# Optimization experiments

Hardware: AMD Instinct MI355X
Metric: run time of the kernel (lower is better)

Reference implementation:

```python
import jax, jax.numpy as jnp
import numpy as np

N = 50000
E = 800000
F_IN = 128
HID = 64
HEADS = 4
P = 16384


def setup_inputs() -> dict:
    key = jax.random.key(0)
    ks = jax.random.split(key, 20)
    s = 0.05
    inp = {
        'x': jax.random.normal(ks[0], (N, F_IN), jnp.float32),
        'edge_src': jax.random.randint(ks[1], (E,), 0, N, jnp.int32),
        'edge_dst': jax.random.randint(ks[2], (E,), 0, N, jnp.int32),
        'edge_attr': jax.random.uniform(ks[3], (E, 1), jnp.float32),
        'pair_indices': jax.random.randint(ks[4], (P, 2), 0, N, jnp.int32),
        # conv1: in=F_IN, heads=4, out=HID, edge_dim=1
        'W1': jax.random.normal(ks[5], (F_IN, HEADS * HID), jnp.float32) * s,
        'We1': jax.random.normal(ks[6], (1, HEADS * HID), jnp.float32) * s,
        'as1': jax.random.normal(ks[7], (HEADS, HID), jnp.float32) * s,
        'ad1': jax.random.normal(ks[8], (HEADS, HID), jnp.float32) * s,
        'ae1': jax.random.normal(ks[9], (HEADS, HID), jnp.float32) * s,
        'b1': jnp.zeros((HEADS * HID,), jnp.float32),
        # conv2: in=4*HID, heads=1, out=HID
        'W2': jax.random.normal(ks[10], (HEADS * HID, HID), jnp.float32) * s,
        'We2': jax.random.normal(ks[11], (1, HID), jnp.float32) * s,
        'as2': jax.random.normal(ks[12], (1, HID), jnp.float32) * s,
        'ad2': jax.random.normal(ks[13], (1, HID), jnp.float32) * s,
        'ae2': jax.random.normal(ks[14], (1, HID), jnp.float32) * s,
        'b2': jnp.zeros((HID,), jnp.float32),
        'Wlin': jax.random.normal(ks[15], (2 * HID, 1), jnp.float32) * s,
        'blin': jnp.zeros((1,), jnp.float32),
    }
    return inp


def gat_conv(x, src, dst, edge_attr, W, We, att_src, att_dst, att_edge, bias, heads, C):
    """PyG GATConv (add_self_loops=True, fill_value='mean', negative_slope=0.2, eval mode)."""
    n = x.shape[0]
    # self-loop edge_attr = mean of incoming edge attrs per node
    deg = jax.ops.segment_sum(jnp.ones_like(dst, dtype=edge_attr.dtype), dst, num_segments=n)
    loop_attr = jax.ops.segment_sum(edge_attr, dst, num_segments=n) / jnp.maximum(deg, 1.0)[:, None]
    loop = jnp.arange(n, dtype=src.dtype)
    src_f = jnp.concatenate([src, loop])
    dst_f = jnp.concatenate([dst, loop])
    ea = jnp.concatenate([edge_attr, loop_attr], axis=0)  # [E+N, 1]
    h = (x @ W).reshape(n, heads, C)                      # [N, H, C]
    a_src = (h * att_src).sum(-1)                         # [N, H]
    a_dst = (h * att_dst).sum(-1)
    e = (ea @ We).reshape(-1, heads, C)                   # [E+N, H, C]
    a_edge = (e * att_edge).sum(-1)                       # [E+N, H]
    alpha = jax.nn.leaky_relu(a_src[src_f] + a_dst[dst_f] + a_edge, 0.2)
    amax = jax.ops.segment_max(alpha, dst_f, num_segments=n)
    ex = jnp.exp(alpha - amax[dst_f])
    denom = jax.ops.segment_sum(ex, dst_f, num_segments=n)
    w = ex / denom[dst_f]                                 # segment softmax over dst
    msg = h[src_f] * w[..., None]                         # [E+N, H, C]
    out = jax.ops.segment_sum(msg, dst_f, num_segments=n) # [N, H, C]
    return out.reshape(n, heads * C) + bias


def reference(x, edge_src, edge_dst, edge_attr, pair_indices,
              W1, We1, as1, ad1, ae1, b1,
              W2, We2, as2, ad2, ae2, b2, Wlin, blin):
    # dropout is identity in eval mode
    h1 = jax.nn.elu(gat_conv(x, edge_src, edge_dst, edge_attr,
                             W1, We1, as1, ad1, ae1, b1, HEADS, HID))
    h2 = gat_conv(h1, edge_src, edge_dst, edge_attr,
                  W2, We2, as2, ad2, ae2, b2, 1, HID)
    d1 = h2[pair_indices[:, 0]]
    d2 = h2[pair_indices[:, 1]]
    pf = jnp.concatenate([d1, d2], axis=1)                # [P, 2*HID]
    return jax.nn.sigmoid(pf @ Wlin + blin).reshape(-1)
```

## Files before the change

kernel.cpp:

```cpp
#include <hip/hip_runtime.h>
#include <hip/hip_fp16.h>
#include <math.h>

typedef __attribute__((ext_vector_type(8))) short short8;
typedef __attribute__((ext_vector_type(4))) float floatx4;
typedef __attribute__((ext_vector_type(2))) float float2v;

#define LOG2E 1.4426950408889634f

__device__ __forceinline__ unsigned short f2bf(float f){
  unsigned int x = __float_as_uint(f);
  unsigned int r = x + 0x7fff + ((x >> 16) & 1);
  return (unsigned short)(r >> 16);
}
__device__ __forceinline__ unsigned cvtpkbf(float lo, float hi){
  unsigned r;
  asm("v_cvt_pk_bf16_f32 %0, %1, %2" : "=v"(r) : "v"(lo), "v"(hi));
  return r;
}
__device__ __forceinline__ short8 pk8(float4 a0, float4 a1){
  unsigned t[4];
  t[0] = cvtpkbf(a0.x, a0.y); t[1] = cvtpkbf(a0.z, a0.w);
  t[2] = cvtpkbf(a1.x, a1.y); t[3] = cvtpkbf(a1.z, a1.w);
  short8 r; __builtin_memcpy(&r, t, 16); return r;
}
__device__ __forceinline__ unsigned char f2fp8(float v){
  int pk = __builtin_amdgcn_cvt_pk_fp8_f32(v, 0.f, 0, false);
  return (unsigned char)(pk & 0xff);
}
__device__ __forceinline__ float wsumf(float v){
#pragma unroll
  for (int o = 32; o; o >>= 1) v += __shfl_xor(v, o, 64);
  return v;
}
__device__ __forceinline__ unsigned pkh2(float a, float b){
  auto p = __builtin_amdgcn_cvt_pkrtz(a, b);
  unsigned u; __builtin_memcpy(&u, &p, 4); return u;
}
__device__ __forceinline__ float h2f(unsigned v){
  unsigned short us = (unsigned short)v;
  __fp16 h; __builtin_memcpy(&h, &us, 2);
  return (float)h;
}

__global__ __launch_bounds__(64) void k_prep(
    const float* __restrict__ W1, const float* __restrict__ as1,
    const float* __restrict__ ad1, const float* __restrict__ W2,
    const float* __restrict__ as2, const float* __restrict__ ad2,
    const float* __restrict__ We1, const float* __restrict__ ae1,
    const float* __restrict__ We2, const float* __restrict__ ae2,
    const float* __restrict__ b2, const float* __restrict__ Wlin,
    unsigned short* __restrict__ W1p, float* __restrict__ w2vT,
    float* __restrict__ ce){
  int b = blockIdx.x, lane = threadIdx.x;
  if (b < 68){
    int nt = b >> 2, kc = b & 3;
    int col = lane & 15, krow = kc * 32 + (lane >> 4) * 8;
    unsigned short tmp[8];
    if (nt < 16){
#pragma unroll
      for (int j = 0; j < 8; j++) tmp[j] = f2bf(W1[(size_t)(krow + j) * 256 + nt * 16 + col]);
    } else {
#pragma unroll
      for (int j = 0; j < 8; j++){
        float v = 0.f;
        if (col < 8){
          const float* av = (col < 4) ? as1 : ad1;
          int h = col & 3;
          for (int c = 0; c < 64; c++)
            v += W1[(size_t)(krow + j) * 256 + h * 64 + c] * av[h * 64 + c];
          v *= LOG2E;
        }
        tmp[j] = f2bf(v);
      }
    }
    unsigned short* dstp = W1p + (((size_t)nt * 4 + kc) * 64 + lane) * 8;
    *(ushort4*)(dstp)     = make_ushort4(tmp[0], tmp[1], tmp[2], tmp[3]);
    *(ushort4*)(dstp + 4) = make_ushort4(tmp[4], tmp[5], tmp[6], tmp[7]);
  } else if (b < 72){
    int k = (b - 68) * 64 + lane;
    float4 a = make_float4(0.f, 0.f, 0.f, 0.f);
    for (int c = 0; c < 64; c++){
      float wv = W2[(size_t)k * 64 + c];
      a.x += wv * as2[c];
      a.y += wv * ad2[c];
      a.z += wv * Wlin[c];
      a.w += wv * Wlin[64 + c];
    }
    w2vT[k]       = a.x * LOG2E;
    w2vT[256 + k] = a.y * LOG2E;
    w2vT[512 + k] = a.z;
    w2vT[768 + k] = a.w;
  } else {
    float p0 = We1[lane]       * ae1[lane];
    float p1 = We1[64 + lane]  * ae1[64 + lane];
    float p2 = We1[128 + lane] * ae1[128 + lane];
    float p3 = We1[192 + lane] * ae1[192 + lane];
    float p4 = We2[lane]       * ae2[lane];
    float c1 = b2[lane] * Wlin[lane];
    float c2 = b2[lane] * Wlin[64 + lane];
    p0 = wsumf(p0); p1 = wsumf(p1); p2 = wsumf(p2); p3 = wsumf(p3); p4 = wsumf(p4);
    c1 = wsumf(c1); c2 = wsumf(c2);
    if (lane == 0){
      ce[0] = p0 * LOG2E; ce[1] = p1 * LOG2E; ce[2] = p2 * LOG2E; ce[3] = p3 * LOG2E;
      ce[4] = p4 * LOG2E;
      ce[5] = c1; ce[6] = c2;
    }
  }
}

__global__ __launch_bounds__(256, 2) void k_count_gemm(
    const int* __restrict__ dst, const float* __restrict__ eattr,
    unsigned* __restrict__ degp, unsigned char* __restrict__ rank,
    int E, int N, int gbl,
    const float* __restrict__ A, const unsigned short* __restrict__ Bp,
    unsigned char* __restrict__ h1f8, float* __restrict__ asrc,
    float* __restrict__ adst, int M){
  __shared__ unsigned short Bs[256 * 64];
  if ((int)blockIdx.x >= gbl){
    int eb = blockIdx.x - gbl;
    int e0 = eb * 512 + threadIdx.x;
    int e1 = e0 + 256;
    bool v0 = e0 < E, v1 = e1 < E;
    int d0 = 0, d1 = 0; float a0 = 0.f, a1 = 0.f;
    if (v0){ d0 = dst[e0]; a0 = eattr[e0]; }
    if (v1){ d1 = dst[e1]; a1 = eattr[e1]; }
    int b0 = (e0 >> 8) & 7, b1 = (e1 >> 8) & 7;
    if (v0){
      unsigned old = atomicAdd(&degp[(size_t)b0 * N + d0],
                               (1u << 24) | (unsigned)(a0 * 262144.0f));
      rank[e0] = (unsigned char)(old >> 24);
    }
    if (v1){
      unsigned old = atomicAdd(&degp[(size_t)b1 * N + d1],
                               (1u << 24) | (unsigned)(a1 * 262144.0f));
      rank[e1] = (unsigned char)(old >> 24);
    }
    return;
  }
  constexpr int K = 128, NKC = 4;
  int wave = threadIdx.x >> 6, lane = threadIdx.x & 63;
  int quad = lane >> 4, col = lane & 15;
  int r0a = blockIdx.x * 128 + wave * 16;
  int r0b = r0a + 64;
  int rowa = min(r0a + col, M - 1);
  int rowb = min(r0b + col, M - 1);
  short8 afa[NKC], afb[NKC], sf[NKC];
#pragma unroll
  for (int kc = 0; kc < NKC; kc++){
    float4 a0 = *(const float4*)(A + (size_t)rowa * K + kc * 32 + quad * 8);
    float4 a1 = *(const float4*)(A + (size_t)rowa * K + kc * 32 + quad * 8 + 4);
    float4 b0 = *(const float4*)(A + (size_t)rowb * K + kc * 32 + quad * 8);
    float4 b1 = *(const float4*)(A + (size_t)rowb * K + kc * 32 + quad * 8 + 4);
    afa[kc] = pk8(a0, a1);
    afb[kc] = pk8(b0, b1);
    sf[kc] = *(const short8*)(Bp + (((size_t)16 * 4 + kc) * 64 + lane) * 8);
  }
  floatx4 acc0[17], acc1[17];
#pragma unroll
  for (int nt = 0; nt < 17; nt++){
    acc0[nt] = (floatx4){0.f, 0.f, 0.f, 0.f};
    acc1[nt] = (floatx4){0.f, 0.f, 0.f, 0.f};
  }
#pragma unroll
  for (int ph = 0; ph < 2; ph++){
    {
      const uint4* srcp = (const uint4*)(Bp + ph * 16384);
      uint4* dstp = (uint4*)Bs;
      for (int i = threadIdx.x; i < 2048; i += 256) dstp[i] = srcp[i];
    }
    __syncthreads();
#pragma unroll
    for (int kc = 0; kc < NKC; kc++){
#pragma unroll
      for (int t = 0; t < 8; t++){
        short8 bfv = *(const short8*)(&Bs[((t * NKC + kc) * 64 + lane) * 8]);
        acc0[ph * 8 + t] = __builtin_amdgcn_mfma_f32_16x16x32_bf16(afa[kc], bfv, acc0[ph * 8 + t], 0, 0, 0);
        acc1[ph * 8 + t] = __builtin_amdgcn_mfma_f32_16x16x32_bf16(afb[kc], bfv, acc1[ph * 8 + t], 0, 0, 0);
      }
    }
    __syncthreads();
  }
#pragma unroll
  for (int kc = 0; kc < NKC; kc++){
    acc0[16] = __builtin_amdgcn_mfma_f32_16x16x32_bf16(afa[kc], sf[kc], acc0[16], 0, 0, 0);
    acc1[16] = __builtin_amdgcn_mfma_f32_16x16x32_bf16(afb[kc], sf[kc], acc1[16], 0, 0, 0);
  }
#pragma unroll
  for (int nt = 0; nt < 16; nt++){
#pragma unroll
    for (int i = 0; i < 4; i++){
      int r = r0a + quad * 4 + i;
      if (r < M) h1f8[(size_t)r * 256 + nt * 16 + col] = f2fp8(acc0[nt][i]);
    }
  }
#pragma unroll
  for (int i = 0; i < 4; i++){
    int r = r0a + quad * 4 + i;
    if (r < M){
      float v = acc0[16][i];
      if (col < 4)      asrc[(size_t)r * 4 + col] = v;
      else if (col < 8) adst[(size_t)r * 4 + (col - 4)] = v;
    }
  }
#pragma unroll
  for (int nt = 0; nt < 16; nt++){
#pragma unroll
    for (int i = 0; i < 4; i++){
      int r = r0b + quad * 4 + i;
      if (r < M) h1f8[(size_t)r * 256 + nt * 16 + col] = f2fp8(acc1[nt][i]);
    }
  }
#pragma unroll
  for (int i = 0; i < 4; i++){
    int r = r0b + quad * 4 + i;
    if (r < M){
      float v = acc1[16][i];
      if (col < 4)      asrc[(size_t)r * 4 + col] = v;
      else if (col < 8) adst[(size_t)r * 4 + (col - 4)] = v;
    }
  }
}

__global__ __launch_bounds__(256) void k_scan1(const unsigned* __restrict__ degp,
    int* __restrict__ row_ptr, int* __restrict__ bsum, int n){
  __shared__ int sm[2][256];
  int tid = threadIdx.x, gid = blockIdx.x * 256 + tid;
  int v = 0;
  if (gid < n){
#pragma unroll
    for (int b = 0; b < 8; b++) v += (int)(degp[(size_t)b * n + gid] >> 24);
  }
  sm[0][tid] = v; __syncthreads();
  int pin = 0;
  for (int off = 1; off < 256; off <<= 1){
    int t = sm[pin][tid];
    if (tid >= off) t += sm[pin][tid - off];
    sm[pin ^ 1][tid] = t; pin ^= 1; __syncthreads();
  }
  int incl = sm[pin][tid];
  if (gid < n) row_ptr[gid] = incl - v;
  if (tid == 255) bsum[blockIdx.x] = incl;
}

__global__ __launch_bounds__(256) void k_scan3(int* __restrict__ row_ptr,
    const int* __restrict__ bsum, const unsigned* __restrict__ degp,
    float* __restrict__ lattr, int* __restrict__ base, int n, int E){
  int tid = threadIdx.x;
  int partial = (tid < (int)blockIdx.x) ? bsum[tid] : 0;
#pragma unroll
  for (int o = 32; o; o >>= 1) partial += __shfl_xor(partial, o, 64);
  __shared__ int ws[4];
  if ((tid & 63) == 0) ws[tid >> 6] = partial;
  __syncthreads();
  int blockOfs = ws[0] + ws[1] + ws[2] + ws[3];
  int gid = blockIdx.x * 256 + tid;
  if (gid >= n) return;
  int rp = row_ptr[gid] + blockOfs;
  row_ptr[gid] = rp;
  int cum = 0; float s = 0.f;
  int bb[8];
#pragma unroll
  for (int b = 0; b < 8; b++){
    unsigned p = degp[(size_t)b * n + gid];
    bb[b] = rp + cum;
    cum += (int)(p >> 24);
    s += (float)(p & 0xffffffu);
  }
  lattr[gid] = (s * (1.0f / 262144.0f)) / fmaxf((float)cum, 1.0f);
  int4* bp = (int4*)(base + (size_t)gid * 8);
  bp[0] = make_int4(bb[0], bb[1], bb[2], bb[3]);
  bp[1] = make_int4(bb[4], bb[5], bb[6], bb[7]);
  if (gid == 0) row_ptr[n] = E;
}

__global__ __launch_bounds__(256) void k_scatter(const int* __restrict__ src,
    const int* __restrict__ dst, const float* __restrict__ eattr,
    const unsigned char* __restrict__ rank, const int* __restrict__ base,
    const float* __restrict__ a_src, int4* __restrict__ csr, int E){
  int e0 = blockIdx.x * 512 + threadIdx.x;
  int e1 = e0 + 256;
  bool v0 = e0 < E, v1 = e1 < E;
  int b0 = (e0 >> 8) & 7, b1 = (e1 >> 8) & 7;
  if (v0){
    int d = dst[e0], s = src[e0];
    int pos = base[(size_t)d * 8 + b0] + (int)rank[e0];
    float4 av = *(const float4*)(a_src + ((size_t)s << 2));
    csr[pos] = make_int4(s, __float_as_int(eattr[e0]),
                         (int)pkh2(av.x, av.y), (int)pkh2(av.z, av.w));
  }
  if (v1){
    int d = dst[e1], s = src[e1];
    int pos = base[(size_t)d * 8 + b1] + (int)rank[e1];
    float4 av = *(const float4*)(a_src + ((size_t)s << 2));
    csr[pos] = make_int4(s, __float_as_int(eattr[e1]),
                         (int)pkh2(av.x, av.y), (int)pkh2(av.z, av.w));
  }
}

__global__ __launch_bounds__(128) void k_gat1(
    const int* __restrict__ row_ptr, const int4* __restrict__ csr,
    const float* __restrict__ lattr,
    const float* __restrict__ a_src, const float* __restrict__ a_dst,
    const float* __restrict__ ce, const unsigned char* __restrict__ hpre,
    const float* __restrict__ bias, const float* __restrict__ w2vT,
    float4* __restrict__ upd, int n){
  int node = blockIdx.x * 2 + (threadIdx.x >> 6);
  if (node >= n) return;
  int lane = threadIdx.x & 63;
  int q = lane >> 4, lsub = lane & 15, hq = lsub >> 2;
  int start = row_ptr[node], deg = row_ptr[node + 1] - start;
  float4 as4 = *(const float4*)(a_src + (size_t)node * 4);
  float4 ad4 = *(const float4*)(a_dst + (size_t)node * 4);
  float4 ce4 = *(const float4*)ce;
  float la = lattr[node];
  float asvh = hq == 0 ? as4.x : hq == 1 ? as4.y : hq == 2 ? as4.z : as4.w;
  float advh = hq == 0 ? ad4.x : hq == 1 ? ad4.y : hq == 2 ? ad4.z : ad4.w;
  float ceh  = hq == 0 ? ce4.x : hq == 1 ? ce4.y : hq == 2 ? ce4.z : ce4.w;
  unsigned lso = (unsigned)(lsub << 4);
  int hsh = (hq & 1) * 16;
  float2v acc2[8];
#pragma unroll
  for (int k = 0; k < 8; k++) acc2[k] = (float2v){0.f, 0.f};
  float dn = 0.f;
  if (q == 0){
    float aself = fmaf(la, ceh, asvh + advh);
    aself = aself > 0.f ? aself : 0.2f * aself;
    float wself = __builtin_amdgcn_exp2f(aself);
    dn = wself;
    uint4 u = *(const uint4*)(hpre + (((unsigned)node << 8) + lso));
    float2v w2 = (float2v){wself, wself};
    unsigned uu[4] = {u.x, u.y, u.z, u.w};
#pragma unroll
    for (int j = 0; j < 4; j++){
      acc2[2 * j]     = w2 * __builtin_amdgcn_cvt_pk_f32_fp8((int)uu[j], false);
      acc2[2 * j + 1] = w2 * __builtin_amdgcn_cvt_pk_f32_fp8((int)uu[j], true);
    }
  }
  int4 sA = make_int4(0, 0, 0, 0), sB;
  if (q < deg) sA = csr[start + q];
  sB = sA;
  if (q + 4 < deg) sB = csr[start + q + 4];
  for (int e = q; e < deg; e += 8){
    uint4 uA = *(const uint4*)(hpre + (((unsigned)sA.x << 8) + lso));
    uint4 uB = *(const uint4*)(hpre + (((unsigned)sB.x << 8) + lso));
    int4 nA = sA, nB;
    int en = e + 8;
    if (en < deg) nA = csr[start + en];
    nB = nA;
    if (en + 4 < deg) nB = csr[start + en + 4];
    bool vB = (e + 4) < deg;
    unsigned hwA = (hq & 2) ? (unsigned)sA.w : (unsigned)sA.z;
    unsigned hwB = (hq & 2) ? (unsigned)sB.w : (unsigned)sB.z;
    float gA = h2f(hwA >> hsh);
    float gB = h2f(hwB >> hsh);
    float aA = fmaf(__int_as_float(sA.y), ceh, gA + advh);
    float aB = fmaf(__int_as_float(sB.y), ceh, gB + advh);
    aA = aA > 0.f ? aA : 0.2f * aA;
    aB = aB > 0.f ? aB : 0.2f * aB;
    float wA = __builtin_amdgcn_exp2f(aA);
    float wB = vB ? __builtin_amdgcn_exp2f(aB) : 0.f;
    dn += wA + wB;
    float2v wA2 = (float2v){wA, wA}, wB2 = (float2v){wB, wB};
    unsigned ua[4] = {uA.x, uA.y, uA.z, uA.w};
    unsigned ub[4] = {uB.x, uB.y, uB.z, uB.w};
#pragma unroll
    for (int j = 0; j < 4; j++){
      acc2[2 * j]     += wA2 * __builtin_amdgcn_cvt_pk_f32_fp8((int)ua[j], false);
      acc2[2 * j + 1] += wA2 * __builtin_amdgcn_cvt_pk_f32_fp8((int)ua[j], true);
      acc2[2 * j]     += wB2 * __builtin_amdgcn_cvt_pk_f32_fp8((int)ub[j], false);
      acc2[2 * j + 1] += wB2 * __builtin_amdgcn_cvt_pk_f32_fp8((int)ub[j], true);
    }
    sA = nA; sB = nB;
  }
  dn += __shfl_xor(dn, 16, 64);
  dn += __shfl_xor(dn, 32, 64);
#pragma unroll
  for (int k = 0; k < 8; k++){
    acc2[k].x += __shfl_xor(acc2[k].x, 16, 64);
    acc2[k].x += __shfl_xor(acc2[k].x, 32, 64);
    acc2[k].y += __shfl_xor(acc2[k].y, 16, 64);
    acc2[k].y += __shfl_xor(acc2[k].y, 32, 64);
  }
  {
    float inv = 1.f / dn;
    float d = 0.f;
#pragma unroll
    for (int j = 0; j < 4; j++){
      float4 b4  = *(const float4*)(bias + lsub * 16 + j * 4);
      float4 wvj = *(const float4*)(w2vT + (size_t)lane * 16 + j * 4);
      float bbv[4] = {b4.x, b4.y, b4.z, b4.w};
      float wvv[4] = {wvj.x, wvj.y, wvj.z, wvj.w};
#pragma unroll
      for (int t = 0; t < 4; t++){
        int k = j * 4 + t;
        float av = (k & 1) ? acc2[k >> 1].y : acc2[k >> 1].x;
        float v = av * inv + bbv[t];
        v = v > 0.f ? v : (__expf(v) - 1.f);
        d += v * wvv[t];
      }
    }
#pragma unroll
    for (int o = 1; o < 16; o <<= 1) d += __shfl_xor(d, o, 64);
    if (lsub == 0) ((float*)&upd[node])[q] = d;
  }
}

__global__ __launch_bounds__(128) void k_gat2(
    const int* __restrict__ row_ptr, const int4* __restrict__ csr,
    const float* __restrict__ lattr, const float4* __restrict__ upd,
    const float* __restrict__ ce,
    float* __restrict__ s1v, float* __restrict__ s2v, int n){
  int node = blockIdx.x * 16 + (threadIdx.x >> 3);
  if (node >= n) return;
  int lane8 = threadIdx.x & 7;
  int start = row_ptr[node], deg = row_ptr[node + 1] - start;
  float4 own = upd[node];
  float ad = own.y, c = ce[4];
  const float* updf = (const float*)upd;
  float t1 = 0.f, t2 = 0.f, dn = 0.f;
  if (lane8 == 0){
    float a = fmaf(lattr[node], c, own.x + ad);
    a = a > 0.f ? a : 0.2f * a;
    float w = __builtin_amdgcn_exp2f(a);
    dn = w; t1 = w * own.z; t2 = w * own.w;
  }
  for (int e = lane8; e < deg; e += 16){
    bool vB = (e + 8) < deg;
    int4 sA = csr[start + e];
    int4 sB = csr[start + (vB ? e + 8 : e)];
    float4 oA = *(const float4*)(updf + ((unsigned)sA.x << 2));
    float4 oB = *(const float4*)(updf + ((unsigned)sB.x << 2));
    float aA = fmaf(__int_as_float(sA.y), c, oA.x + ad);
    float aB = fmaf(__int_as_float(sB.y), c, oB.x + ad);
    aA = aA > 0.f ? aA : 0.2f * aA;
    aB = aB > 0.f ? aB : 0.2f * aB;
    float wA = __builtin_amdgcn_exp2f(aA);
    float wB = vB ? __builtin_amdgcn_exp2f(aB) : 0.f;
    dn += wA + wB;
    t1 = fmaf(wA, oA.z, fmaf(wB, oB.z, t1));
    t2 = fmaf(wA, oA.w, fmaf(wB, oB.w, t2));
  }
#pragma unroll
  for (int o = 1; o < 8; o <<= 1){
    dn += __shfl_xor(dn, o, 64);
    t1 += __shfl_xor(t1, o, 64);
    t2 += __shfl_xor(t2, o, 64);
  }
  if (lane8 == 0){
    float inv = 1.f / dn;
    s1v[node] = t1 * inv + ce[5];
    s2v[node] = t2 * inv + ce[6];
  }
}

__global__ __launch_bounds__(256) void k_pairs(const int* __restrict__ pairs,
    const float* __restrict__ s1v, const float* __restrict__ s2v,
    const float* __restrict__ blin, float* __restrict__ out, int P){
  int p = blockIdx.x * 256 + threadIdx.x;
  if (p >= P) return;
  int i = pairs[2 * p], j = pairs[2 * p + 1];
  float x = s1v[i] + s2v[j] + blin[0];
  out[p] = 1.f / (1.f + __expf(-x));
}

extern "C" void kernel_launch(void* const* d_in, const int* in_sizes, int n_in,
                              void* d_out, int out_size, void* d_ws, size_t ws_size,
                              hipStream_t stream) {
  const float* x     = (const float*)d_in[0];
  const int*   esrc  = (const int*)  d_in[1];
  const int*   edst  = (const int*)  d_in[2];
  const float* eattr = (const float*)d_in[3];
  const int*   pairs = (const int*)  d_in[4];
  const float* W1    = (const float*)d_in[5];
  const float* We1   = (const float*)d_in[6];
  const float* as1   = (const float*)d_in[7];
  const float* ad1   = (const float*)d_in[8];
  const float* ae1   = (const float*)d_in[9];
  const float* b1    = (const float*)d_in[10];
  const float* W2    = (const float*)d_in[11];
  const float* We2   = (const float*)d_in[12];
  const float* as2   = (const float*)d_in[13];
  const float* ad2   = (const float*)d_in[14];
  const float* ae2   = (const float*)d_in[15];
  const float* b2    = (const float*)d_in[16];
  const float* Wlin  = (const float*)d_in[17];
  const float* blin  = (const float*)d_in[18];
  float* out = (float*)d_out;

  const int N = in_sizes[0] / 128;
  const int E = in_sizes[1];
  const int P = in_sizes[4] / 2;

  char* w = (char*)d_ws;
  size_t off = 0;
  auto alloc = [&](size_t bytes) -> size_t {
    size_t r = off; off = (off + bytes + 255) & ~(size_t)255; return r;
  };
  size_t o_degp   = alloc((size_t)N * 32);
  size_t zero_end = off;
  size_t o_rank   = alloc((size_t)E);
  size_t o_rowptr = alloc((size_t)(N + 1) * 4);
  size_t o_bsum   = alloc(1024);
  size_t o_lattr  = alloc((size_t)N * 4);
  size_t o_base   = alloc((size_t)N * 32);
  size_t o_csr    = alloc((size_t)E * 16);
  size_t o_asrc1  = alloc((size_t)N * 16);
  size_t o_adst1  = alloc((size_t)N * 16);
  size_t o_upd    = alloc((size_t)N * 16);
  size_t o_ce     = alloc(64);
  size_t o_s1     = alloc((size_t)N * 4);
  size_t o_s2     = alloc((size_t)N * 4);
  size_t o_W1p    = alloc((size_t)17 * 4 * 64 * 8 * 2);
  size_t o_w2v    = alloc(256 * 16);
  size_t o_h1f8   = alloc((size_t)N * 256);
  (void)ws_size;

  unsigned* degp = (unsigned*)(w + o_degp);
  unsigned char* rank = (unsigned char*)(w + o_rank);
  int*   rowptr = (int*)  (w + o_rowptr);
  int*   bsum   = (int*)  (w + o_bsum);
  float* lattr  = (float*)(w + o_lattr);
  int*   base   = (int*)  (w + o_base);
  int4*  csr    = (int4*) (w + o_csr);
  float* asrc1  = (float*)(w + o_asrc1);
  float* adst1  = (float*)(w + o_adst1);
  float4* upd   = (float4*)(w + o_upd);
  float* ce     = (float*)(w + o_ce);
  float* s1v    = (float*)(w + o_s1);
  float* s2v    = (float*)(w + o_s2);
  unsigned short* W1p = (unsigned short*)(w + o_W1p);
  float* w2vT   = (float*)(w + o_w2v);
  unsigned char* h1f8 = (unsigned char*)(w + o_h1f8);

  (void)hipMemsetAsync(w, 0, zero_end, stream);

  int ebl2 = (E + 511) / 512;
  int nbl = (N + 255) / 256;
  int gbl = (N + 127) / 128;
  int wbl = (N + 1) / 2;

  k_prep<<<73, 64, 0, stream>>>(W1, as1, ad1, W2, as2, ad2,
                                We1, ae1, We2, ae2, b2, Wlin, W1p, w2vT, ce);
  k_count_gemm<<<gbl + ebl2, 256, 0, stream>>>(edst, eattr, degp, rank, E, N, gbl,
      x, W1p, h1f8, asrc1, adst1, N);
  k_scan1<<<nbl, 256, 0, stream>>>(degp, rowptr, bsum, N);
  k_scan3<<<nbl, 256, 0, stream>>>(rowptr, bsum, degp, lattr, base, N, E);
  k_scatter<<<ebl2, 256, 0, stream>>>(esrc, edst, eattr, rank, base, asrc1, csr, E);
  k_gat1<<<wbl, 128, 0, stream>>>(rowptr, csr, lattr, asrc1, adst1, ce,
                                  h1f8, b1, w2vT, upd, N);
  k_gat2<<<(N + 15) / 16, 128, 0, stream>>>(rowptr, csr, lattr, upd, ce,
                                            s1v, s2v, N);
  k_pairs<<<(P + 255) / 256, 256, 0, stream>>>(pairs, s1v, s2v, blin, out, P);
}
```

Measured before the change: 237.1 us.

## Split GAT layer-1 aggregation per head with compact per-head CSR entries

The scatter pass now writes a head-major CSR of 4-byte entries per head. Each entry packs a 16-bit source index with an fp16 precomputed edge logit (a_src plus edge-attr times the attention coefficient). It also writes a separate compact CSR for layer 2. The layer-1 kernel launches four times as many blocks, one set per head, so each wave gathers only a 64-byte slice of the fp8 features and keeps far fewer accumulators, and results are combined with atomicAdd into a now-zeroed output buffer. This is meant to cut per-edge metadata traffic and register pressure and raise parallelism. The costs are atomics, loss of the explicit next-edge prefetch, fp16 rounding of logits, and a hard limit of N below 65536.

```diff
diff --git a/kernel.cpp b/kernel.cpp
--- a/kernel.cpp
+++ b/kernel.cpp
@@ -277,137 +277,110 @@
 __global__ __launch_bounds__(256) void k_scatter(const int* __restrict__ src,
     const int* __restrict__ dst, const float* __restrict__ eattr,
     const unsigned char* __restrict__ rank, const int* __restrict__ base,
-    const float* __restrict__ a_src, int4* __restrict__ csr, int E){
+    const float* __restrict__ a_src, const float* __restrict__ ce,
+    unsigned* __restrict__ csrh, unsigned* __restrict__ csr2, int E){
+  float4 ce4 = *(const float4*)ce;
+  float ce5 = ce[4];
   int e0 = blockIdx.x * 512 + threadIdx.x;
-  int e1 = e0 + 256;
-  bool v0 = e0 < E, v1 = e1 < E;
-  int b0 = (e0 >> 8) & 7, b1 = (e1 >> 8) & 7;
-  if (v0){
-    int d = dst[e0], s = src[e0];
-    int pos = base[(size_t)d * 8 + b0] + (int)rank[e0];
+#pragma unroll
+  for (int t = 0; t < 2; t++){
+    int e = e0 + t * 256;
+    if (e >= E) break;
+    int d = dst[e], s = src[e];
+    int b = (e >> 8) & 7;
+    int pos = base[(size_t)d * 8 + b] + (int)rank[e];
     float4 av = *(const float4*)(a_src + ((size_t)s << 2));
-    csr[pos] = make_int4(s, __float_as_int(eattr[e0]),
-                         (int)pkh2(av.x, av.y), (int)pkh2(av.z, av.w));
-  }
-  if (v1){
-    int d = dst[e1], s = src[e1];
-    int pos = base[(size_t)d * 8 + b1] + (int)rank[e1];
-    float4 av = *(const float4*)(a_src + ((size_t)s << 2));
-    csr[pos] = make_int4(s, __float_as_int(eattr[e1]),
-                         (int)pkh2(av.x, av.y), (int)pkh2(av.z, av.w));
-  }
-}
-
-__global__ __launch_bounds__(128) void k_gat1(
-    const int* __restrict__ row_ptr, const int4* __restrict__ csr,
+    float ea = eattr[e];
+    unsigned su = (unsigned)s;
+    csrh[pos]                 = su | (pkh2(fmaf(ea, ce4.x, av.x), 0.f) << 16);
+    csrh[(size_t)E + pos]     = su | (pkh2(fmaf(ea, ce4.y, av.y), 0.f) << 16);
+    csrh[(size_t)2 * E + pos] = su | (pkh2(fmaf(ea, ce4.z, av.z), 0.f) << 16);
+    csrh[(size_t)3 * E + pos] = su | (pkh2(fmaf(ea, ce4.w, av.w), 0.f) << 16);
+    csr2[pos]                 = su | (pkh2(ea * ce5, 0.f) << 16);
+  }
+}
+
+__global__ __launch_bounds__(128) void k_gat1h(
+    const int* __restrict__ row_ptr, const unsigned* __restrict__ csrh,
     const float* __restrict__ lattr,
     const float* __restrict__ a_src, const float* __restrict__ a_dst,
     const float* __restrict__ ce, const unsigned char* __restrict__ hpre,
-    const float* __restrict__ bias, const float* __restrict__ w2vT,
-    float4* __restrict__ upd, int n){
-  int node = blockIdx.x * 2 + (threadIdx.x >> 6);
+    const float* __restrict__ b1, const float* __restrict__ w2vT,
+    float* __restrict__ updf, int n, int E, int wbl){
+  int h = blockIdx.x / wbl;
+  int nb = blockIdx.x - h * wbl;
+  int node = nb * 2 + (threadIdx.x >> 6);
   if (node >= n) return;
   int lane = threadIdx.x & 63;
-  int q = lane >> 4, lsub = lane & 15, hq = lsub >> 2;
+  int q = lane >> 4, lsub = lane & 15;
   int start = row_ptr[node], deg = row_ptr[node + 1] - start;
-  float4 as4 = *(const float4*)(a_src + (size_t)node * 4);
-  float4 ad4 = *(const float4*)(a_dst + (size_t)node * 4);
-  float4 ce4 = *(const float4*)ce;
+  float asvh = a_src[(size_t)node * 4 + h];
+  float advh = a_dst[(size_t)node * 4 + h];
+  float ceh = ce[h];
   float la = lattr[node];
-  float asvh = hq == 0 ? as4.x : hq == 1 ? as4.y : hq == 2 ? as4.z : as4.w;
-  float advh = hq == 0 ? ad4.x : hq == 1 ? ad4.y : hq == 2 ? ad4.z : ad4.w;
-  float ceh  = hq == 0 ? ce4.x : hq == 1 ? ce4.y : hq == 2 ? ce4.z : ce4.w;
-  unsigned lso = (unsigned)(lsub << 4);
-  int hsh = (hq & 1) * 16;
-  float2v acc2[8];
-#pragma unroll
-  for (int k = 0; k < 8; k++) acc2[k] = (float2v){0.f, 0.f};
+  const unsigned* cs = csrh + (size_t)h * E + start;
+  unsigned fo = ((unsigned)h << 6) + ((unsigned)lsub << 2);
+  float2v acc0 = (float2v){0.f, 0.f}, acc1 = (float2v){0.f, 0.f};
   float dn = 0.f;
   if (q == 0){
     float aself = fmaf(la, ceh, asvh + advh);
     aself = aself > 0.f ? aself : 0.2f * aself;
-    float wself = __builtin_amdgcn_exp2f(aself);
-    dn = wself;
-    uint4 u = *(const uint4*)(hpre + (((unsigned)node << 8) + lso));
-    float2v w2 = (float2v){wself, wself};
-    unsigned uu[4] = {u.x, u.y, u.z, u.w};
-#pragma unroll
-    for (int j = 0; j < 4; j++){
-      acc2[2 * j]     = w2 * __builtin_amdgcn_cvt_pk_f32_fp8((int)uu[j], false);
-      acc2[2 * j + 1] = w2 * __builtin_amdgcn_cvt_pk_f32_fp8((int)uu[j], true);
-    }
-  }
-  int4 sA = make_int4(0, 0, 0, 0), sB;
-  if (q < deg) sA = csr[start + q];
-  sB = sA;
-  if (q + 4 < deg) sB = csr[start + q + 4];
+    float ws = __builtin_amdgcn_exp2f(aself);
+    dn = ws;
+    unsigned u = *(const unsigned*)(hpre + (((unsigned)node << 8) + fo));
+    float2v w2 = (float2v){ws, ws};
+    acc0 = w2 * __builtin_amdgcn_cvt_pk_f32_fp8((int)u, false);
+    acc1 = w2 * __builtin_amdgcn_cvt_pk_f32_fp8((int)u, true);
+  }
   for (int e = q; e < deg; e += 8){
-    uint4 uA = *(const uint4*)(hpre + (((unsigned)sA.x << 8) + lso));
-    uint4 uB = *(const uint4*)(hpre + (((unsigned)sB.x << 8) + lso));
-    int4 nA = sA, nB;
-    int en = e + 8;
-    if (en < deg) nA = csr[start + en];
-    nB = nA;
-    if (en + 4 < deg) nB = csr[start + en + 4];
     bool vB = (e + 4) < deg;
-    unsigned hwA = (hq & 2) ? (unsigned)sA.w : (unsigned)sA.z;
-    unsigned hwB = (hq & 2) ? (unsigned)sB.w : (unsigned)sB.z;
-    float gA = h2f(hwA >> hsh);
-    float gB = h2f(hwB >> hsh);
-    float aA = fmaf(__int_as_float(sA.y), ceh, gA + advh);
-    float aB = fmaf(__int_as_float(sB.y), ceh, gB + advh);
+    unsigned A = cs[e];
+    unsigned B = cs[vB ? e + 4 : e];
+    unsigned uA = *(const unsigned*)(hpre + (((A & 0xffffu) << 8) + fo));
+    unsigned uB = *(const unsigned*)(hpre + (((B & 0xffffu) << 8) + fo));
+    float aA = h2f(A >> 16) + advh;
+    float aB = h2f(B >> 16) + advh;
     aA = aA > 0.f ? aA : 0.2f * aA;
     aB = aB > 0.f ? aB : 0.2f * aB;
     float wA = __builtin_amdgcn_exp2f(aA);
     float wB = vB ? __builtin_amdgcn_exp2f(aB) : 0.f;
     dn += wA + wB;
     float2v wA2 = (float2v){wA, wA}, wB2 = (float2v){wB, wB};
-    unsigned ua[4] = {uA.x, uA.y, uA.z, uA.w};
-    unsigned ub[4] = {uB.x, uB.y, uB.z, uB.w};
-#pragma unroll
-    for (int j = 0; j < 4; j++){
-      acc2[2 * j]     += wA2 * __builtin_amdgcn_cvt_pk_f32_fp8((int)ua[j], false);
-      acc2[2 * j + 1] += wA2 * __builtin_amdgcn_cvt_pk_f32_fp8((int)ua[j], true);
-      acc2[2 * j]     += wB2 * __builtin_amdgcn_cvt_pk_f32_fp8((int)ub[j], false);
-      acc2[2 * j + 1] += wB2 * __builtin_amdgcn_cvt_pk_f32_fp8((int)ub[j], true);
-    }
-    sA = nA; sB = nB;
+    acc0 += wA2 * __builtin_amdgcn_cvt_pk_f32_fp8((int)uA, false);
+    acc1 += wA2 * __builtin_amdgcn_cvt_pk_f32_fp8((int)uA, true);
+    acc0 += wB2 * __builtin_amdgcn_cvt_pk_f32_fp8((int)uB, false);
+    acc1 += wB2 * __builtin_amdgcn_cvt_pk_f32_fp8((int)uB, true);
   }
   dn += __shfl_xor(dn, 16, 64);
   dn += __shfl_xor(dn, 32, 64);
-#pragma unroll
-  for (int k = 0; k < 8; k++){
-    acc2[k].x += __shfl_xor(acc2[k].x, 16, 64);
-    acc2[k].x += __shfl_xor(acc2[k].x, 32, 64);
-    acc2[k].y += __shfl_xor(acc2[k].y, 16, 64);
-    acc2[k].y += __shfl_xor(acc2[k].y, 32, 64);
-  }
+  float v0 = acc0.x, v1 = acc0.y, v2 = acc1.x, v3 = acc1.y;
+  v0 += __shfl_xor(v0, 16, 64); v0 += __shfl_xor(v0, 32, 64);
+  v1 += __shfl_xor(v1, 16, 64); v1 += __shfl_xor(v1, 32, 64);
+  v2 += __shfl_xor(v2, 16, 64); v2 += __shfl_xor(v2, 32, 64);
+  v3 += __shfl_xor(v3, 16, 64); v3 += __shfl_xor(v3, 32, 64);
   {
     float inv = 1.f / dn;
+    unsigned gf = ((unsigned)h << 6) + ((unsigned)lsub << 2);
+    float4 b4 = *(const float4*)(b1 + gf);
+    float4 wv = *(const float4*)(w2vT + (size_t)q * 256 + gf);
+    float vv[4] = {v0, v1, v2, v3};
+    float bb[4] = {b4.x, b4.y, b4.z, b4.w};
+    float ww[4] = {wv.x, wv.y, wv.z, wv.w};
     float d = 0.f;
 #pragma unroll
     for (int j = 0; j < 4; j++){
-      float4 b4  = *(const float4*)(bias + lsub * 16 + j * 4);
-      float4 wvj = *(const float4*)(w2vT + (size_t)lane * 16 + j * 4);
-      float bbv[4] = {b4.x, b4.y, b4.z, b4.w};
-      float wvv[4] = {wvj.x, wvj.y, wvj.z, wvj.w};
-#pragma unroll
-      for (int t = 0; t < 4; t++){
-        int k = j * 4 + t;
-        float av = (k & 1) ? acc2[k >> 1].y : acc2[k >> 1].x;
-        float v = av * inv + bbv[t];
-        v = v > 0.f ? v : (__expf(v) - 1.f);
-        d += v * wvv[t];
-      }
+      float v = vv[j] * inv + bb[j];
+      v = v > 0.f ? v : (__expf(v) - 1.f);
+      d += v * ww[j];
     }
 #pragma unroll
     for (int o = 1; o < 16; o <<= 1) d += __shfl_xor(d, o, 64);
-    if (lsub == 0) ((float*)&upd[node])[q] = d;
+    if (lsub == 0) atomicAdd(&updf[(size_t)node * 4 + q], d);
   }
 }
 
 __global__ __launch_bounds__(128) void k_gat2(
-    const int* __restrict__ row_ptr, const int4* __restrict__ csr,
+    const int* __restrict__ row_ptr, const unsigned* __restrict__ csr2,
     const float* __restrict__ lattr, const float4* __restrict__ upd,
     const float* __restrict__ ce,
     float* __restrict__ s1v, float* __restrict__ s2v, int n){
@@ -427,12 +400,12 @@
   }
   for (int e = lane8; e < deg; e += 16){
     bool vB = (e + 8) < deg;
-    int4 sA = csr[start + e];
-    int4 sB = csr[start + (vB ? e + 8 : e)];
-    float4 oA = *(const float4*)(updf + ((unsigned)sA.x << 2));
-    float4 oB = *(const float4*)(updf + ((unsigned)sB.x << 2));
-    float aA = fmaf(__int_as_float(sA.y), c, oA.x + ad);
-    float aB = fmaf(__int_as_float(sB.y), c, oB.x + ad);
+    unsigned sA = csr2[start + e];
+    unsigned sB = csr2[start + (vB ? e + 8 : e)];
+    float4 oA = *(const float4*)(updf + ((sA & 0xffffu) << 2));
+    float4 oB = *(const float4*)(updf + ((sB & 0xffffu) << 2));
+    float aA = oA.x + ad + h2f(sA >> 16);
+    float aB = oB.x + ad + h2f(sB >> 16);
     aA = aA > 0.f ? aA : 0.2f * aA;
     aB = aB > 0.f ? aB : 0.2f * aB;
     float wA = __builtin_amdgcn_exp2f(aA);
@@ -498,16 +471,17 @@
     size_t r = off; off = (off + bytes + 255) & ~(size_t)255; return r;
   };
   size_t o_degp   = alloc((size_t)N * 32);
+  size_t o_upd    = alloc((size_t)N * 16);
   size_t zero_end = off;
   size_t o_rank   = alloc((size_t)E);
   size_t o_rowptr = alloc((size_t)(N + 1) * 4);
   size_t o_bsum   = alloc(1024);
   size_t o_lattr  = alloc((size_t)N * 4);
   size_t o_base   = alloc((size_t)N * 32);
-  size_t o_csr    = alloc((size_t)E * 16);
+  size_t o_csrh   = alloc((size_t)E * 16);
+  size_t o_csr2   = alloc((size_t)E * 4);
   size_t o_asrc1  = alloc((size_t)N * 16);
   size_t o_adst1  = alloc((size_t)N * 16);
-  size_t o_upd    = alloc((size_t)N * 16);
   size_t o_ce     = alloc(64);
   size_t o_s1     = alloc((size_t)N * 4);
   size_t o_s2     = alloc((size_t)N * 4);
@@ -517,15 +491,16 @@
   (void)ws_size;
 
   unsigned* degp = (unsigned*)(w + o_degp);
+  float4* upd   = (float4*)(w + o_upd);
   unsigned char* rank = (unsigned char*)(w + o_rank);
   int*   rowptr = (int*)  (w + o_rowptr);
   int*   bsum   = (int*)  (w + o_bsum);
   float* lattr  = (float*)(w + o_lattr);
   int*   base   = (int*)  (w + o_base);
-  int4*  csr    = (int4*) (w + o_csr);
+  unsigned* csrh = (unsigned*)(w + o_csrh);
+  unsigned* csr2 = (unsigned*)(w + o_csr2);
   float* asrc1  = (float*)(w + o_asrc1);
   float* adst1  = (float*)(w + o_adst1);
-  float4* upd   = (float4*)(w + o_upd);
   float* ce     = (float*)(w + o_ce);
   float* s1v    = (float*)(w + o_s1);
   float* s2v    = (float*)(w + o_s2);
@@ -546,10 +521,11 @@
       x, W1p, h1f8, asrc1, adst1, N);
   k_scan1<<<nbl, 256, 0, stream>>>(degp, rowptr, bsum, N);
   k_scan3<<<nbl, 256, 0, stream>>>(rowptr, bsum, degp, lattr, base, N, E);
-  k_scatter<<<ebl2, 256, 0, stream>>>(esrc, edst, eattr, rank, base, asrc1, csr, E);
-  k_gat1<<<wbl, 128, 0, stream>>>(rowptr, csr, lattr, asrc1, adst1, ce,
-                                  h1f8, b1, w2vT, upd, N);
-  k_gat2<<<(N + 15) / 16, 128, 0, stream>>>(rowptr, csr, lattr, upd, ce,
+  k_scatter<<<ebl2, 256, 0, stream>>>(esrc, edst, eattr, rank, base, asrc1, ce,
+                                      csrh, csr2, E);
+  k_gat1h<<<4 * wbl, 128, 0, stream>>>(rowptr, csrh, lattr, asrc1, adst1, ce,
+                                       h1f8, b1, w2vT, (float*)upd, N, E, wbl);
+  k_gat2<<<(N + 15) / 16, 128, 0, stream>>>(rowptr, csr2, lattr, upd, ce,
                                             s1v, s2v, N);
   k_pairs<<<(P + 255) / 256, 256, 0, stream>>>(pairs, s1v, s2v, blin, out, P);
 }
```

Result: slower. 317.6 us (+33.9%).

## Replace two-pass scan with single-pass atomic block allocation of CSR ranges

Applied to the files above, without the earlier changes.

Merges the two scan kernels into one that reserves each block's edge range with a global atomicAdd instead of a second pass over block sums. CSR rows are no longer globally ordered by node, so a per-node degree array replaces row_ptr[n+1] differences in both GAT kernels. This drops one kernel launch and a re-read of the degree partials. In exchange the edge ordering across blocks becomes nondeterministic and the consumers do an extra degree load.

```diff
diff --git a/kernel.cpp b/kernel.cpp
--- a/kernel.cpp
+++ b/kernel.cpp
@@ -222,14 +222,21 @@
   }
 }
 
-__global__ __launch_bounds__(256) void k_scan1(const unsigned* __restrict__ degp,
-    int* __restrict__ row_ptr, int* __restrict__ bsum, int n){
+__global__ __launch_bounds__(256) void k_scanf(const unsigned* __restrict__ degp,
+    unsigned* __restrict__ gcur, int* __restrict__ rowstart,
+    int* __restrict__ degv, float* __restrict__ lattr,
+    int* __restrict__ base, int n){
   __shared__ int sm[2][256];
+  __shared__ int bbase;
   int tid = threadIdx.x, gid = blockIdx.x * 256 + tid;
+  unsigned p[8];
   int v = 0;
   if (gid < n){
 #pragma unroll
-    for (int b = 0; b < 8; b++) v += (int)(degp[(size_t)b * n + gid] >> 24);
+    for (int b = 0; b < 8; b++){
+      p[b] = degp[(size_t)b * n + gid];
+      v += (int)(p[b] >> 24);
+    }
   }
   sm[0][tid] = v; __syncthreads();
   int pin = 0;
@@ -239,39 +246,24 @@
     sm[pin ^ 1][tid] = t; pin ^= 1; __syncthreads();
   }
   int incl = sm[pin][tid];
-  if (gid < n) row_ptr[gid] = incl - v;
-  if (tid == 255) bsum[blockIdx.x] = incl;
-}
-
-__global__ __launch_bounds__(256) void k_scan3(int* __restrict__ row_ptr,
-    const int* __restrict__ bsum, const unsigned* __restrict__ degp,
-    float* __restrict__ lattr, int* __restrict__ base, int n, int E){
-  int tid = threadIdx.x;
-  int partial = (tid < (int)blockIdx.x) ? bsum[tid] : 0;
-#pragma unroll
-  for (int o = 32; o; o >>= 1) partial += __shfl_xor(partial, o, 64);
-  __shared__ int ws[4];
-  if ((tid & 63) == 0) ws[tid >> 6] = partial;
+  if (tid == 255) bbase = (int)atomicAdd(gcur, (unsigned)incl);
   __syncthreads();
-  int blockOfs = ws[0] + ws[1] + ws[2] + ws[3];
-  int gid = blockIdx.x * 256 + tid;
   if (gid >= n) return;
-  int rp = row_ptr[gid] + blockOfs;
-  row_ptr[gid] = rp;
+  int rp = bbase + incl - v;
+  rowstart[gid] = rp;
+  degv[gid] = v;
   int cum = 0; float s = 0.f;
   int bb[8];
 #pragma unroll
   for (int b = 0; b < 8; b++){
-    unsigned p = degp[(size_t)b * n + gid];
     bb[b] = rp + cum;
-    cum += (int)(p >> 24);
-    s += (float)(p & 0xffffffu);
+    cum += (int)(p[b] >> 24);
+    s += (float)(p[b] & 0xffffffu);
   }
   lattr[gid] = (s * (1.0f / 262144.0f)) / fmaxf((float)cum, 1.0f);
   int4* bp = (int4*)(base + (size_t)gid * 8);
   bp[0] = make_int4(bb[0], bb[1], bb[2], bb[3]);
   bp[1] = make_int4(bb[4], bb[5], bb[6], bb[7]);
-  if (gid == 0) row_ptr[n] = E;
 }
 
 __global__ __launch_bounds__(256) void k_scatter(const int* __restrict__ src,
@@ -299,8 +291,8 @@
 }
 
 __global__ __launch_bounds__(128) void k_gat1(
-    const int* __restrict__ row_ptr, const int4* __restrict__ csr,
-    const float* __restrict__ lattr,
+    const int* __restrict__ rowstart, const int* __restrict__ degv,
+    const int4* __restrict__ csr, const float* __restrict__ lattr,
     const float* __restrict__ a_src, const float* __restrict__ a_dst,
     const float* __restrict__ ce, const unsigned char* __restrict__ hpre,
     const float* __restrict__ bias, const float* __restrict__ w2vT,
@@ -309,7 +301,7 @@
   if (node >= n) return;
   int lane = threadIdx.x & 63;
   int q = lane >> 4, lsub = lane & 15, hq = lsub >> 2;
-  int start = row_ptr[node], deg = row_ptr[node + 1] - start;
+  int start = rowstart[node], deg = degv[node];
   float4 as4 = *(const float4*)(a_src + (size_t)node * 4);
   float4 ad4 = *(const float4*)(a_dst + (size_t)node * 4);
   float4 ce4 = *(const float4*)ce;
@@ -407,14 +399,14 @@
 }
 
 __global__ __launch_bounds__(128) void k_gat2(
-    const int* __restrict__ row_ptr, const int4* __restrict__ csr,
-    const float* __restrict__ lattr, const float4* __restrict__ upd,
-    const float* __restrict__ ce,
+    const int* __restrict__ rowstart, const int* __restrict__ degv,
+    const int4* __restrict__ csr, const float* __restrict__ lattr,
+    const float4* __restrict__ upd, const float* __restrict__ ce,
     float* __restrict__ s1v, float* __restrict__ s2v, int n){
   int node = blockIdx.x * 16 + (threadIdx.x >> 3);
   if (node >= n) return;
   int lane8 = threadIdx.x & 7;
-  int start = row_ptr[node], deg = row_ptr[node + 1] - start;
+  int start = rowstart[node], deg = degv[node];
   float4 own = upd[node];
   float ad = own.y, c = ce[4];
   const float* updf = (const float*)upd;
@@ -498,10 +490,11 @@
     size_t r = off; off = (off + bytes + 255) & ~(size_t)255; return r;
   };
   size_t o_degp   = alloc((size_t)N * 32);
+  size_t o_gcur   = alloc(256);
   size_t zero_end = off;
   size_t o_rank   = alloc((size_t)E);
-  size_t o_rowptr = alloc((size_t)(N + 1) * 4);
-  size_t o_bsum   = alloc(1024);
+  size_t o_rowst  = alloc((size_t)N * 4);
+  size_t o_degv   = alloc((size_t)N * 4);
   size_t o_lattr  = alloc((size_t)N * 4);
   size_t o_base   = alloc((size_t)N * 32);
   size_t o_csr    = alloc((size_t)E * 16);
@@ -517,9 +510,10 @@
   (void)ws_size;
 
   unsigned* degp = (unsigned*)(w + o_degp);
+  unsigned* gcur = (unsigned*)(w + o_gcur);
   unsigned char* rank = (unsigned char*)(w + o_rank);
-  int*   rowptr = (int*)  (w + o_rowptr);
-  int*   bsum   = (int*)  (w + o_bsum);
+  int*   rowst  = (int*)  (w + o_rowst);
+  int*   degv   = (int*)  (w + o_degv);
   float* lattr  = (float*)(w + o_lattr);
   int*   base   = (int*)  (w + o_base);
   int4*  csr    = (int4*) (w + o_csr);
@@ -544,12 +538,11 @@
                                 We1, ae1, We2, ae2, b2, Wlin, W1p, w2vT, ce);
   k_count_gemm<<<gbl + ebl2, 256, 0, stream>>>(edst, eattr, degp, rank, E, N, gbl,
       x, W1p, h1f8, asrc1, adst1, N);
-  k_scan1<<<nbl, 256, 0, stream>>>(degp, rowptr, bsum, N);
-  k_scan3<<<nbl, 256, 0, stream>>>(rowptr, bsum, degp, lattr, base, N, E);
+  k_scanf<<<nbl, 256, 0, stream>>>(degp, gcur, rowst, degv, lattr, base, N);
   k_scatter<<<ebl2, 256, 0, stream>>>(esrc, edst, eattr, rank, base, asrc1, csr, E);
-  k_gat1<<<wbl, 128, 0, stream>>>(rowptr, csr, lattr, asrc1, adst1, ce,
+  k_gat1<<<wbl, 128, 0, stream>>>(rowst, degv, csr, lattr, asrc1, adst1, ce,
                                   h1f8, b1, w2vT, upd, N);
-  k_gat2<<<(N + 15) / 16, 128, 0, stream>>>(rowptr, csr, lattr, upd, ce,
+  k_gat2<<<(N + 15) / 16, 128, 0, stream>>>(rowst, degv, csr, lattr, upd, ce,
                                             s1v, s2v, N);
   k_pairs<<<(P + 255) / 256, 256, 0, stream>>>(pairs, s1v, s2v, blin, out, P);
 }
```

New measurement: 237.0 us. Within noise of the previous version (-0.0%).
